# Kernel optimization log

Hardware: AMD Instinct MI355X
Metric: run time of the kernel (lower is better)

## Reference

```python
import jax, jax.numpy as jnp
import numpy as np

EMBED_DIM = 1024
NUM_HEADS = 16
HEAD_DIM = EMBED_DIM // NUM_HEADS


def setup_inputs() -> dict:
    key = jax.random.key(0)
    k1, k2, k3, k4, k5 = jax.random.split(key, 5)
    s = 1.0 / np.sqrt(EMBED_DIM)
    return {
        "query": jax.random.normal(k1, (8, 1024, EMBED_DIM), dtype=jnp.float32),
        "w_qkv": jax.random.normal(k2, (EMBED_DIM, 3 * EMBED_DIM), dtype=jnp.float32) * s,
        "b_qkv": jax.random.normal(k3, (3 * EMBED_DIM,), dtype=jnp.float32) * 0.01,
        "w_proj": jax.random.normal(k4, (EMBED_DIM, EMBED_DIM), dtype=jnp.float32) * s,
        "b_proj": jax.random.normal(k5, (EMBED_DIM,), dtype=jnp.float32) * 0.01,
    }


def reference(query, w_qkv, b_qkv, w_proj, b_proj):
    B, S, D = query.shape
    H, Hd = NUM_HEADS, HEAD_DIM
    scale = 1.0 / jnp.sqrt(jnp.asarray(Hd, query.dtype))
    # fused QKV projection; key=value=query (self-attention), so one GEMM suffices
    qkv = query @ w_qkv + b_qkv                      # [B, S, 3D]
    qkv = qkv.reshape(B, S, 3, H, Hd)
    q = qkv[:, :, 0].transpose(0, 2, 1, 3)           # [B, H, S, Hd]
    k = qkv[:, :, 1].transpose(0, 2, 1, 3)
    v = qkv[:, :, 2].transpose(0, 2, 1, 3)
    attn = jnp.einsum("bhqd,bhkd->bhqk", q, k) * scale
    attn = jax.nn.softmax(attn, axis=-1)
    out = jnp.einsum("bhqk,bhkd->bhqd", attn, v)     # [B, H, S, Hd]
    out = out.transpose(0, 2, 1, 3).reshape(B, S, D)
    return out @ w_proj + b_proj
```

## Files before the change

### kernel.cpp

```cpp
#include <hip/hip_runtime.h>
#include <stdint.h>

#define DEV __device__ __forceinline__

typedef short bf16x8 __attribute__((ext_vector_type(8)));
typedef float f32x4 __attribute__((ext_vector_type(4)));
typedef float f32x16 __attribute__((ext_vector_type(16)));
typedef unsigned u32x2 __attribute__((ext_vector_type(2)));

DEV short f2bf(float f) {
  uint32_t x = __builtin_bit_cast(uint32_t, f);
  uint32_t r = x + 0x7fffu + ((x >> 16) & 1u);
  return (short)(r >> 16);
}

DEV unsigned cvtpk(float lo, float hi) {
  unsigned r;
  asm("v_cvt_pk_bf16_f32 %0, %1, %2" : "=v"(r) : "v"(lo), "v"(hi));
  return r;
}
DEV void pswap(unsigned& a, unsigned& b) {
  asm("v_permlane32_swap_b32 %0, %1" : "+v"(a), "+v"(b));
}

DEV void gld16(const short* g, short* l) {
  __builtin_amdgcn_global_load_lds(
      (const __attribute__((address_space(1))) void*)g,
      (__attribute__((address_space(3))) void*)l, 16, 0, 0);
}

__global__ __launch_bounds__(256) void k_cvt(const float* __restrict__ in,
                                             short* __restrict__ out, int n8) {
  int i = blockIdx.x * 256 + threadIdx.x;
  if (i >= n8) return;
  const float4* p = (const float4*)in + (size_t)i * 2;
  float4 a = p[0], b = p[1];
  bf16x8 v;
  v[0] = f2bf(a.x); v[1] = f2bf(a.y); v[2] = f2bf(a.z); v[3] = f2bf(a.w);
  v[4] = f2bf(b.x); v[5] = f2bf(b.y); v[6] = f2bf(b.z); v[7] = f2bf(b.w);
  *(bf16x8*)(out + (size_t)i * 8) = v;
}

__global__ __launch_bounds__(256) void k_tcvt(const float* __restrict__ in,
                                              short* __restrict__ out, int K, int N) {
  __shared__ float tile[64][65];
  int t = threadIdx.x;
  int n0 = blockIdx.x * 64, k0 = blockIdx.y * 64;
  int kl = t >> 4, nl = (t & 15) * 4;
#pragma unroll
  for (int it = 0; it < 4; ++it) {
    float4 v = *(const float4*)&in[(size_t)(k0 + kl + it * 16) * N + n0 + nl];
    tile[nl + 0][kl + it * 16] = v.x;
    tile[nl + 1][kl + it * 16] = v.y;
    tile[nl + 2][kl + it * 16] = v.z;
    tile[nl + 3][kl + it * 16] = v.w;
  }
  __syncthreads();
  int no = t >> 2, kc = (t & 3) * 16;
  bf16x8 v0, v1;
#pragma unroll
  for (int c = 0; c < 8; ++c) v0[c] = f2bf(tile[no][kc + c]);
#pragma unroll
  for (int c = 0; c < 8; ++c) v1[c] = f2bf(tile[no][kc + 8 + c]);
  size_t ob = (size_t)(n0 + no) * K + k0 + kc;
  *(bf16x8*)&out[ob] = v0;
  *(bf16x8*)&out[ob + 8] = v1;
}

__global__ __launch_bounds__(256) void k_vt(const short* __restrict__ vin,
                                            short* __restrict__ vt) {
  __shared__ alignas(16) short tile[64][72];
  int t = threadIdx.x;
  int sc = blockIdx.x, bh = blockIdx.y;
  int sl = t >> 3, dc = (t & 7) * 8;
  const short* base = vin + ((size_t)bh * 1024 + sc * 64) * 64;
#pragma unroll
  for (int it = 0; it < 2; ++it)
    *(bf16x8*)&tile[sl + it * 32][dc] = *(const bf16x8*)&base[(size_t)(sl + it * 32) * 64 + dc];
  __syncthreads();
  int d = t >> 2, s2 = (t & 3) * 16;
  bf16x8 v0, v1;
#pragma unroll
  for (int c = 0; c < 8; ++c) v0[c] = tile[s2 + c][d];
#pragma unroll
  for (int c = 0; c < 8; ++c) v1[c] = tile[s2 + 8 + c][d];
  size_t ob = (size_t)bh * 65536 + (size_t)d * 1024 + sc * 64 + s2;
  *(bf16x8*)&vt[ob] = v0;
  *(bf16x8*)&vt[ob + 8] = v1;
}

template <int MODE, int BN>
__global__ __launch_bounds__(256) void k_gemm(const short* __restrict__ A,
                                              const short* __restrict__ Bw,
                                              const float* __restrict__ bias,
                                              void* o0, void* o1, void* o2) {
  constexpr int JN = BN / 32;
  __shared__ alignas(16) short lA[128 * 64];
  __shared__ alignas(16) short lB[BN * 64];
  int t = threadIdx.x;
  int w = t >> 6, l = t & 63;
  int wr = w >> 1, wc = w & 1;
  int lr = l & 15, lg = l >> 4;

  int nbx = gridDim.x;
  int flat = blockIdx.y * nbx + blockIdx.x;
  int tot = nbx * gridDim.y;
  int swz = (flat & 7) * (tot >> 3) + (flat >> 3);
  int m0 = (swz / nbx) * 128, n0 = (swz % nbx) * BN;

  f32x4 acc[4][JN] = {};

  int srow = t >> 3;
  int schunk = (t & 7) ^ (srow & 7);
  const short* ap = A + (size_t)(m0 + srow) * 1024 + schunk * 8;
  const short* bp = Bw + (size_t)(n0 + srow) * 1024 + schunk * 8;
  short* la0 = &lA[w * 512];
  short* lb0 = &lB[w * 512];

  for (int k0 = 0; k0 < 1024; k0 += 64) {
#pragma unroll
    for (int c = 0; c < 4; ++c)
      gld16(ap + (size_t)c * 32 * 1024 + k0, la0 + c * 2048);
#pragma unroll
    for (int c = 0; c < JN; ++c)
      gld16(bp + (size_t)c * 32 * 1024 + k0, lb0 + c * 2048);
    __syncthreads();
    bf16x8 af[4][2], bfr[JN][2];
#pragma unroll
    for (int i = 0; i < 4; ++i)
#pragma unroll
      for (int ks = 0; ks < 2; ++ks) {
        int ra = wr * 64 + i * 16 + lr;
        af[i][ks] = *(const bf16x8*)&lA[ra * 64 + (((ks * 4 + lg) ^ (ra & 7)) * 8)];
      }
#pragma unroll
    for (int j = 0; j < JN; ++j)
#pragma unroll
      for (int ks = 0; ks < 2; ++ks) {
        int rb = wc * (BN / 2) + j * 16 + lr;
        bfr[j][ks] = *(const bf16x8*)&lB[rb * 64 + (((ks * 4 + lg) ^ (rb & 7)) * 8)];
      }
#pragma unroll
    for (int i = 0; i < 4; ++i)
#pragma unroll
      for (int j = 0; j < JN; ++j)
#pragma unroll
        for (int ks = 0; ks < 2; ++ks)
          acc[i][j] = __builtin_amdgcn_mfma_f32_16x16x32_bf16(af[i][ks], bfr[j][ks], acc[i][j], 0, 0, 0);
    __syncthreads();
  }

  if (MODE == 0) {
    short* outs[3] = {(short*)o0, (short*)o1, (short*)o2};
#pragma unroll
    for (int i = 0; i < 4; ++i)
#pragma unroll
      for (int j = 0; j < JN; ++j) {
        int nn0 = n0 + wc * (BN / 2) + j * 16;
        int sel = nn0 >> 10;
        short* op = outs[sel];
        float qs = (sel == 0) ? 0.18033688011112042f : 1.0f;
#pragma unroll
        for (int r = 0; r < 4; ++r) {
          int mm = m0 + wr * 64 + i * 16 + lg * 4 + r;
          int nn = nn0 + lr;
          float val = (acc[i][j][r] + bias[nn]) * qs;
          int hh = (nn >> 6) & 15, dd = nn & 63;
          int bb = mm >> 10, ss = mm & 1023;
          op[((size_t)(bb * 16 + hh) * 1024 + ss) * 64 + dd] = f2bf(val);
        }
      }
  } else {
    float* op = (float*)o0;
#pragma unroll
    for (int i = 0; i < 4; ++i)
#pragma unroll
      for (int j = 0; j < JN; ++j)
#pragma unroll
        for (int r = 0; r < 4; ++r) {
          int mm = m0 + wr * 64 + i * 16 + lg * 4 + r;
          int nn = n0 + wc * (BN / 2) + j * 16 + lr;
          op[(size_t)mm * 1024 + nn] = acc[i][j][r] + bias[nn];
        }
  }
}

__global__ __launch_bounds__(256, 4) void k_attn(const short* __restrict__ qb,
                                                 const short* __restrict__ kb,
                                                 const short* __restrict__ vt,
                                                 short* __restrict__ ao) {
  __shared__ alignas(16) short lds[2 * 8192];
  int t = threadIdx.x, w = t >> 6, l = t & 63;
  int r0 = l & 31, hi = l >> 5;

  int bid = blockIdx.x;
  int swz = (bid & 7) * 128 + (bid >> 3);
  int bh = swz >> 3, qc = swz & 7;
  int q0 = qc * 128 + w * 32;

  const short* qbase = qb + (size_t)bh * 65536;
  const short* kbase = kb + (size_t)bh * 65536;
  const short* vbase = vt + (size_t)bh * 65536;

  bf16x8 qf[4];
#pragma unroll
  for (int step = 0; step < 4; ++step)
    qf[step] = *(const bf16x8*)&qbase[(size_t)(q0 + r0) * 64 + step * 16 + hi * 8];

  f32x16 acc0 = {0,0,0,0,0,0,0,0,0,0,0,0,0,0,0,0};
  f32x16 acc1 = {0,0,0,0,0,0,0,0,0,0,0,0,0,0,0,0};
  float ls = 0.f;

  int srow = t >> 3;
  int sch = (t & 7) ^ (srow & 7);
  const short* kp = kbase + (size_t)srow * 64 + sch * 8;
  const short* vp = vbase + (size_t)srow * 1024 + sch * 8;

#define STAGE(buf, kv0)                                              \
  do {                                                               \
    short* dk = &lds[(buf) * 8192 + w * 512];                        \
    short* dv = &lds[(buf) * 8192 + 4096 + w * 512];                 \
    gld16(kp + (size_t)(kv0) * 64, dk);                              \
    gld16(kp + (size_t)((kv0) + 32) * 64, dk + 2048);                \
    gld16(vp + (kv0), dv);                                           \
    gld16(vp + (kv0) + 32 * 1024, dv + 2048);                        \
  } while (0)

  STAGE(0, 0);
  int cur = 0;
  for (int it = 0; it < 16; ++it) {
    __syncthreads();
    if (it < 15) STAGE(cur ^ 1, (it + 1) * 64);
    const short* lk = &lds[cur * 8192];
    const short* lv = &lds[cur * 8192 + 4096];

    f32x16 s0 = {0,0,0,0,0,0,0,0,0,0,0,0,0,0,0,0};
    f32x16 s1 = {0,0,0,0,0,0,0,0,0,0,0,0,0,0,0,0};
    __builtin_amdgcn_s_setprio(1);
#pragma unroll
    for (int step = 0; step < 4; ++step) {
      int ck = step * 2 + hi;
      bf16x8 kf0 = *(const bf16x8*)&lk[r0 * 64 + ((ck ^ (r0 & 7)) * 8)];
      int r1 = 32 + r0;
      bf16x8 kf1 = *(const bf16x8*)&lk[r1 * 64 + ((ck ^ (r1 & 7)) * 8)];
      s0 = __builtin_amdgcn_mfma_f32_32x32x16_bf16(kf0, qf[step], s0, 0, 0, 0);
      s1 = __builtin_amdgcn_mfma_f32_32x32x16_bf16(kf1, qf[step], s1, 0, 0, 0);
    }
    __builtin_amdgcn_s_setprio(0);

    float rs = 0.f;
#pragma unroll
    for (int r = 0; r < 16; ++r) { float p = __builtin_exp2f(s0[r]); s0[r] = p; rs += p; }
#pragma unroll
    for (int r = 0; r < 16; ++r) { float p = __builtin_exp2f(s1[r]); s1[r] = p; rs += p; }
    rs += __shfl_xor(rs, 32);
    ls += rs;

    __builtin_amdgcn_s_setprio(1);
#pragma unroll
    for (int tt = 0; tt < 2; ++tt) {
#pragma unroll
      for (int ks = 0; ks < 2; ++ks) {
        unsigned Aw, Bw2, Cw, Dw;
        if (tt == 0) {
          Aw = cvtpk(s0[8 * ks + 0], s0[8 * ks + 1]);
          Bw2 = cvtpk(s0[8 * ks + 4], s0[8 * ks + 5]);
          Cw = cvtpk(s0[8 * ks + 2], s0[8 * ks + 3]);
          Dw = cvtpk(s0[8 * ks + 6], s0[8 * ks + 7]);
        } else {
          Aw = cvtpk(s1[8 * ks + 0], s1[8 * ks + 1]);
          Bw2 = cvtpk(s1[8 * ks + 4], s1[8 * ks + 5]);
          Cw = cvtpk(s1[8 * ks + 2], s1[8 * ks + 3]);
          Dw = cvtpk(s1[8 * ks + 6], s1[8 * ks + 7]);
        }
        pswap(Aw, Bw2);
        pswap(Cw, Dw);
        union { unsigned u[4]; bf16x8 v; } pb;
        pb.u[0] = Aw; pb.u[1] = Cw; pb.u[2] = Bw2; pb.u[3] = Dw;
        int cv = tt * 4 + ks * 2 + hi;
        bf16x8 vf0 = *(const bf16x8*)&lv[r0 * 64 + ((cv ^ (r0 & 7)) * 8)];
        int r1 = 32 + r0;
        bf16x8 vf1 = *(const bf16x8*)&lv[r1 * 64 + ((cv ^ (r1 & 7)) * 8)];
        acc0 = __builtin_amdgcn_mfma_f32_32x32x16_bf16(vf0, pb.v, acc0, 0, 0, 0);
        acc1 = __builtin_amdgcn_mfma_f32_32x32x16_bf16(vf1, pb.v, acc1, 0, 0, 0);
      }
    }
    __builtin_amdgcn_s_setprio(0);
    cur ^= 1;
  }
#undef STAGE

  __syncthreads();
  short* ep = &lds[w * 2048];
  float inv = 1.0f / ls;
#pragma unroll
  for (int d0 = 0; d0 < 2; ++d0) {
#pragma unroll
    for (int q4 = 0; q4 < 4; ++q4) {
      unsigned w0, w1;
      if (d0 == 0) {
        w0 = cvtpk(acc0[q4 * 4 + 0] * inv, acc0[q4 * 4 + 1] * inv);
        w1 = cvtpk(acc0[q4 * 4 + 2] * inv, acc0[q4 * 4 + 3] * inv);
      } else {
        w0 = cvtpk(acc1[q4 * 4 + 0] * inv, acc1[q4 * 4 + 1] * inv);
        w1 = cvtpk(acc1[q4 * 4 + 2] * inv, acc1[q4 * 4 + 3] * inv);
      }
      int chunk = (q4 + 4 * d0) ^ (r0 & 7);
      u32x2 uv; uv[0] = w0; uv[1] = w1;
      *(u32x2*)((char*)ep + r0 * 128 + chunk * 16 + hi * 8) = uv;
    }
  }
  int b = bh >> 4, hh = bh & 15;
#pragma unroll
  for (int rr = 0; rr < 4; ++rr) {
    int row = (l >> 3) + rr * 8;
    int c = (l & 7) ^ (row & 7);
    bf16x8 ov = *(const bf16x8*)((char*)ep + row * 128 + c * 16);
    int tok = b * 1024 + q0 + row;
    *(bf16x8*)&ao[(size_t)tok * 1024 + hh * 64 + (l & 7) * 8] = ov;
  }
}

extern "C" void kernel_launch(void* const* d_in, const int* in_sizes, int n_in,
                              void* d_out, int out_size, void* d_ws, size_t ws_size,
                              hipStream_t stream) {
  const float* query  = (const float*)d_in[0];
  const float* w_qkv  = (const float*)d_in[1];
  const float* b_qkv  = (const float*)d_in[2];
  const float* w_proj = (const float*)d_in[3];
  const float* b_proj = (const float*)d_in[4];
  float* out = (float*)d_out;
  char* ws = (char*)d_ws;

  short* qbf = (short*)(ws);
  short* wT  = (short*)(ws + 16777216);
  short* wpT = (short*)(ws + 23068672);
  short* qb  = (short*)(ws + 25165824);
  short* kb  = (short*)(ws + 41943040);
  short* vb  = (short*)(ws + 58720256);
  short* vt  = (short*)(ws + 75497472);
  short* ao  = qbf;

  k_cvt<<<4096, 256, 0, stream>>>(query, qbf, 1048576);
  k_tcvt<<<dim3(48, 16), 256, 0, stream>>>(w_qkv, wT, 1024, 3072);
  k_tcvt<<<dim3(16, 16), 256, 0, stream>>>(w_proj, wpT, 1024, 1024);
  k_gemm<0, 96><<<dim3(32, 64), 256, 0, stream>>>(qbf, wT, b_qkv, qb, kb, vb);
  k_vt<<<dim3(16, 128), 256, 0, stream>>>(vb, vt);
  k_attn<<<1024, 256, 0, stream>>>(qb, kb, vt, ao);
  k_gemm<1, 128><<<dim3(8, 64), 256, 0, stream>>>(ao, wpT, b_proj, out, nullptr, nullptr);
}
```

Baseline: 178.8 us.

## Replace QKV GEMM with 256x256-tile 8-wave double-buffered pipelined kernel

Adds a new QKV projection kernel that uses 256x256 output tiles, 512 threads (8 waves) and double-buffered LDS. Global-to-LDS loads for the next K tile are interleaved with four MFMA phases, using explicit waitcnt, barriers and setprio. The larger tile increases operand reuse per byte loaded and the schedule is meant to hide load latency. The cost is 128KB of LDS per block, heavy register pressure from 128 accumulators, a smaller grid of 384 blocks, and a scalar bf16 epilogue store scattered per element.

```diff
diff --git a/kernel.cpp b/kernel.cpp
--- a/kernel.cpp
+++ b/kernel.cpp
@@ -87,6 +87,137 @@
   size_t ob = (size_t)bh * 65536 + (size_t)d * 1024 + sc * 64 + s2;
   *(bf16x8*)&vt[ob] = v0;
   *(bf16x8*)&vt[ob + 8] = v1;
+}
+
+__global__ __launch_bounds__(512, 2) void k_g8(const short* __restrict__ A,
+                                               const short* __restrict__ Bw,
+                                               const float* __restrict__ bias,
+                                               short* __restrict__ oq,
+                                               short* __restrict__ ok,
+                                               short* __restrict__ ov) {
+  __shared__ alignas(16) short lA[2][16384];
+  __shared__ alignas(16) short lB[2][16384];
+  int t = threadIdx.x;
+  int w = t >> 6, l = t & 63;
+  int wr = w >> 2, wc = w & 3;
+  int lr = l & 15, lg = l >> 4;
+
+  int nbx = gridDim.x;
+  int flat = blockIdx.y * nbx + blockIdx.x;
+  int tot = nbx * gridDim.y;
+  int swz = (flat & 7) * (tot >> 3) + (flat >> 3);
+  int m0 = (swz / nbx) * 256, n0 = (swz % nbx) * 256;
+
+  f32x4 acc[8][4] = {};
+
+  int srow = t >> 3;
+  int schunk = (t & 7) ^ (srow & 7);
+  const short* ap = A + (size_t)(m0 + srow) * 1024 + schunk * 8;
+  const short* bp = Bw + (size_t)(n0 + srow) * 1024 + schunk * 8;
+  int lofs = w * 512;
+
+#define SA8(buf, kt, c) gld16(ap + (size_t)(c) * 65536 + (kt) * 64, &lA[buf][(c) * 4096 + lofs])
+#define SB8(buf, kt, c) gld16(bp + (size_t)(c) * 65536 + (kt) * 64, &lB[buf][(c) * 4096 + lofs])
+#define BAR8() do { __builtin_amdgcn_sched_barrier(0); __builtin_amdgcn_s_barrier(); \
+                    __builtin_amdgcn_sched_barrier(0); } while (0)
+#define LGKM0() do { asm volatile("s_waitcnt lgkmcnt(0)" ::: "memory"); \
+                     __builtin_amdgcn_sched_barrier(0); } while (0)
+
+  SB8(0, 0, 0); SB8(0, 0, 1); SB8(0, 0, 2); SB8(0, 0, 3);
+  SA8(0, 0, 0); SA8(0, 0, 2); SA8(0, 0, 1); SA8(0, 0, 3);
+  asm volatile("s_waitcnt vmcnt(2)" ::: "memory");
+  BAR8();
+
+#pragma unroll 2
+  for (int kt = 0; kt < 16; ++kt) {
+    int b = kt & 1;
+    const short* la = lA[b];
+    const short* lb = lB[b];
+    bool st = kt < 15;
+    bf16x8 bfr[4][2], af[2][2];
+
+#define DSREAD_A(p)                                                                     \
+    _Pragma("unroll") for (int i2 = 0; i2 < 2; ++i2)                                    \
+      _Pragma("unroll") for (int ks = 0; ks < 2; ++ks) {                                \
+        int ra = wr * 128 + ((p) * 2 + i2) * 16 + lr;                                   \
+        af[i2][ks] = *(const bf16x8*)&la[ra * 64 + (((ks * 4 + lg) ^ (ra & 7)) * 8)];   \
+      }
+#define MFMA16(p)                                                                       \
+    __builtin_amdgcn_s_setprio(1);                                                      \
+    _Pragma("unroll") for (int i2 = 0; i2 < 2; ++i2)                                    \
+      _Pragma("unroll") for (int nj = 0; nj < 4; ++nj)                                  \
+        _Pragma("unroll") for (int ks = 0; ks < 2; ++ks)                                \
+          acc[(p) * 2 + i2][nj] = __builtin_amdgcn_mfma_f32_16x16x32_bf16(              \
+              af[i2][ks], bfr[nj][ks], acc[(p) * 2 + i2][nj], 0, 0, 0);                 \
+    __builtin_amdgcn_s_setprio(0);
+
+#pragma unroll
+    for (int nj = 0; nj < 4; ++nj)
+#pragma unroll
+      for (int ks = 0; ks < 2; ++ks) {
+        int rb = wc * 64 + nj * 16 + lr;
+        bfr[nj][ks] = *(const bf16x8*)&lb[rb * 64 + (((ks * 4 + lg) ^ (rb & 7)) * 8)];
+      }
+    DSREAD_A(0)
+    if (st) { SB8(b ^ 1, kt + 1, 0); SB8(b ^ 1, kt + 1, 1); }
+    BAR8();
+    LGKM0();
+    MFMA16(0)
+    BAR8();
+
+    DSREAD_A(1)
+    if (st) {
+      SB8(b ^ 1, kt + 1, 2); SB8(b ^ 1, kt + 1, 3);
+      asm volatile("s_waitcnt vmcnt(4)" ::: "memory");
+    } else {
+      asm volatile("s_waitcnt vmcnt(0)" ::: "memory");
+    }
+    BAR8();
+    LGKM0();
+    MFMA16(1)
+    BAR8();
+
+    DSREAD_A(2)
+    if (st) { SA8(b ^ 1, kt + 1, 0); SA8(b ^ 1, kt + 1, 2); }
+    BAR8();
+    LGKM0();
+    MFMA16(2)
+    BAR8();
+
+    DSREAD_A(3)
+    if (st) {
+      SA8(b ^ 1, kt + 1, 1); SA8(b ^ 1, kt + 1, 3);
+      asm volatile("s_waitcnt vmcnt(2)" ::: "memory");
+    }
+    BAR8();
+    LGKM0();
+    MFMA16(3)
+    BAR8();
+#undef DSREAD_A
+#undef MFMA16
+  }
+#undef SA8
+#undef SB8
+
+  short* outs[3] = {oq, ok, ov};
+#pragma unroll
+  for (int mi = 0; mi < 8; ++mi)
+#pragma unroll
+    for (int nj = 0; nj < 4; ++nj) {
+      int nn0 = n0 + wc * 64 + nj * 16;
+      int sel = nn0 >> 10;
+      short* op = outs[sel];
+      float qs = (sel == 0) ? 0.18033688011112042f : 1.0f;
+#pragma unroll
+      for (int r = 0; r < 4; ++r) {
+        int mm = m0 + wr * 128 + mi * 16 + lg * 4 + r;
+        int nn = nn0 + lr;
+        float val = (acc[mi][nj][r] + bias[nn]) * qs;
+        int hh = (nn >> 6) & 15, dd = nn & 63;
+        int bb = mm >> 10, ss = mm & 1023;
+        op[((size_t)(bb * 16 + hh) * 1024 + ss) * 64 + dd] = f2bf(val);
+      }
+    }
 }
 
 template <int MODE, int BN>
@@ -344,7 +475,7 @@
   k_cvt<<<4096, 256, 0, stream>>>(query, qbf, 1048576);
   k_tcvt<<<dim3(48, 16), 256, 0, stream>>>(w_qkv, wT, 1024, 3072);
   k_tcvt<<<dim3(16, 16), 256, 0, stream>>>(w_proj, wpT, 1024, 1024);
-  k_gemm<0, 96><<<dim3(32, 64), 256, 0, stream>>>(qbf, wT, b_qkv, qb, kb, vb);
+  k_g8<<<dim3(12, 32), 512, 0, stream>>>(qbf, wT, b_qkv, qb, kb, vb);
   k_vt<<<dim3(16, 128), 256, 0, stream>>>(vb, vt);
   k_attn<<<1024, 256, 0, stream>>>(qb, kb, vt, ao);
   k_gemm<1, 128><<<dim3(8, 64), 256, 0, stream>>>(ao, wpT, b_proj, out, nullptr, nullptr);
```

New measurement: 182.9 us. 2.3% more time.

## Process two 32-row query tiles per wave in attention kernel with 128-thread blocks

Applied to the files above, without the earlier changes.

The attention block now uses 2 waves instead of 4, and each wave handles 64 query rows as two 32-row tiles. Each K/V fragment read from LDS then feeds twice as many MFMAs, which halves LDS read traffic per unit of compute. Each thread stages more K/V chunks per tile. The cost is roughly double the accumulator and score registers per wave, with fewer waves per block and lower occupancy, so less latency hiding.

```diff
diff --git a/kernel.cpp b/kernel.cpp
--- a/kernel.cpp
+++ b/kernel.cpp
@@ -185,7 +185,7 @@
   }
 }
 
-__global__ __launch_bounds__(256, 4) void k_attn(const short* __restrict__ qb,
+__global__ __launch_bounds__(128, 2) void k_attn(const short* __restrict__ qb,
                                                  const short* __restrict__ kb,
                                                  const short* __restrict__ vt,
                                                  short* __restrict__ ao) {
@@ -196,34 +196,36 @@
   int bid = blockIdx.x;
   int swz = (bid & 7) * 128 + (bid >> 3);
   int bh = swz >> 3, qc = swz & 7;
-  int q0 = qc * 128 + w * 32;
+  int q0 = qc * 128 + w * 64;
 
   const short* qbase = qb + (size_t)bh * 65536;
   const short* kbase = kb + (size_t)bh * 65536;
   const short* vbase = vt + (size_t)bh * 65536;
 
-  bf16x8 qf[4];
-#pragma unroll
-  for (int step = 0; step < 4; ++step)
-    qf[step] = *(const bf16x8*)&qbase[(size_t)(q0 + r0) * 64 + step * 16 + hi * 8];
-
-  f32x16 acc0 = {0,0,0,0,0,0,0,0,0,0,0,0,0,0,0,0};
-  f32x16 acc1 = {0,0,0,0,0,0,0,0,0,0,0,0,0,0,0,0};
-  float ls = 0.f;
-
-  int srow = t >> 3;
-  int sch = (t & 7) ^ (srow & 7);
+  bf16x8 qf[2][4];
+#pragma unroll
+  for (int qt = 0; qt < 2; ++qt)
+#pragma unroll
+    for (int step = 0; step < 4; ++step)
+      qf[qt][step] = *(const bf16x8*)&qbase[(size_t)(q0 + qt * 32 + r0) * 64 + step * 16 + hi * 8];
+
+  f32x16 acc[2][2] = {};
+  float ls[2] = {0.f, 0.f};
+
+  int srow = 32 * w + (l >> 3);
+  int sch = (l & 7) ^ (srow & 7);
   const short* kp = kbase + (size_t)srow * 64 + sch * 8;
   const short* vp = vbase + (size_t)srow * 1024 + sch * 8;
 
-#define STAGE(buf, kv0)                                              \
-  do {                                                               \
-    short* dk = &lds[(buf) * 8192 + w * 512];                        \
-    short* dv = &lds[(buf) * 8192 + 4096 + w * 512];                 \
-    gld16(kp + (size_t)(kv0) * 64, dk);                              \
-    gld16(kp + (size_t)((kv0) + 32) * 64, dk + 2048);                \
-    gld16(vp + (kv0), dv);                                           \
-    gld16(vp + (kv0) + 32 * 1024, dv + 2048);                        \
+#define STAGE(buf, kv0)                                                        \
+  do {                                                                         \
+    short* dk = &lds[(buf) * 8192 + w * 2048];                                 \
+    short* dv = &lds[(buf) * 8192 + 4096 + w * 2048];                          \
+    _Pragma("unroll")                                                          \
+    for (int c = 0; c < 4; ++c) {                                              \
+      gld16(kp + (size_t)((kv0) + 8 * c) * 64, dk + c * 512);                  \
+      gld16(vp + (kv0) + (size_t)(8 * c) * 1024, dv + c * 512);                \
+    }                                                                          \
   } while (0)
 
   STAGE(0, 0);
@@ -234,8 +236,7 @@
     const short* lk = &lds[cur * 8192];
     const short* lv = &lds[cur * 8192 + 4096];
 
-    f32x16 s0 = {0,0,0,0,0,0,0,0,0,0,0,0,0,0,0,0};
-    f32x16 s1 = {0,0,0,0,0,0,0,0,0,0,0,0,0,0,0,0};
+    f32x16 s0[2] = {}, s1[2] = {};
     __builtin_amdgcn_s_setprio(1);
 #pragma unroll
     for (int step = 0; step < 4; ++step) {
@@ -243,46 +244,55 @@
       bf16x8 kf0 = *(const bf16x8*)&lk[r0 * 64 + ((ck ^ (r0 & 7)) * 8)];
       int r1 = 32 + r0;
       bf16x8 kf1 = *(const bf16x8*)&lk[r1 * 64 + ((ck ^ (r1 & 7)) * 8)];
-      s0 = __builtin_amdgcn_mfma_f32_32x32x16_bf16(kf0, qf[step], s0, 0, 0, 0);
-      s1 = __builtin_amdgcn_mfma_f32_32x32x16_bf16(kf1, qf[step], s1, 0, 0, 0);
+#pragma unroll
+      for (int qt = 0; qt < 2; ++qt) {
+        s0[qt] = __builtin_amdgcn_mfma_f32_32x32x16_bf16(kf0, qf[qt][step], s0[qt], 0, 0, 0);
+        s1[qt] = __builtin_amdgcn_mfma_f32_32x32x16_bf16(kf1, qf[qt][step], s1[qt], 0, 0, 0);
+      }
     }
     __builtin_amdgcn_s_setprio(0);
 
-    float rs = 0.f;
-#pragma unroll
-    for (int r = 0; r < 16; ++r) { float p = __builtin_exp2f(s0[r]); s0[r] = p; rs += p; }
-#pragma unroll
-    for (int r = 0; r < 16; ++r) { float p = __builtin_exp2f(s1[r]); s1[r] = p; rs += p; }
-    rs += __shfl_xor(rs, 32);
-    ls += rs;
+#pragma unroll
+    for (int qt = 0; qt < 2; ++qt) {
+      float rs = 0.f;
+#pragma unroll
+      for (int r = 0; r < 16; ++r) { float p = __builtin_exp2f(s0[qt][r]); s0[qt][r] = p; rs += p; }
+#pragma unroll
+      for (int r = 0; r < 16; ++r) { float p = __builtin_exp2f(s1[qt][r]); s1[qt][r] = p; rs += p; }
+      rs += __shfl_xor(rs, 32);
+      ls[qt] += rs;
+    }
 
     __builtin_amdgcn_s_setprio(1);
 #pragma unroll
     for (int tt = 0; tt < 2; ++tt) {
 #pragma unroll
       for (int ks = 0; ks < 2; ++ks) {
-        unsigned Aw, Bw2, Cw, Dw;
-        if (tt == 0) {
-          Aw = cvtpk(s0[8 * ks + 0], s0[8 * ks + 1]);
-          Bw2 = cvtpk(s0[8 * ks + 4], s0[8 * ks + 5]);
-          Cw = cvtpk(s0[8 * ks + 2], s0[8 * ks + 3]);
-          Dw = cvtpk(s0[8 * ks + 6], s0[8 * ks + 7]);
-        } else {
-          Aw = cvtpk(s1[8 * ks + 0], s1[8 * ks + 1]);
-          Bw2 = cvtpk(s1[8 * ks + 4], s1[8 * ks + 5]);
-          Cw = cvtpk(s1[8 * ks + 2], s1[8 * ks + 3]);
-          Dw = cvtpk(s1[8 * ks + 6], s1[8 * ks + 7]);
-        }
-        pswap(Aw, Bw2);
-        pswap(Cw, Dw);
-        union { unsigned u[4]; bf16x8 v; } pb;
-        pb.u[0] = Aw; pb.u[1] = Cw; pb.u[2] = Bw2; pb.u[3] = Dw;
         int cv = tt * 4 + ks * 2 + hi;
         bf16x8 vf0 = *(const bf16x8*)&lv[r0 * 64 + ((cv ^ (r0 & 7)) * 8)];
         int r1 = 32 + r0;
         bf16x8 vf1 = *(const bf16x8*)&lv[r1 * 64 + ((cv ^ (r1 & 7)) * 8)];
-        acc0 = __builtin_amdgcn_mfma_f32_32x32x16_bf16(vf0, pb.v, acc0, 0, 0, 0);
-        acc1 = __builtin_amdgcn_mfma_f32_32x32x16_bf16(vf1, pb.v, acc1, 0, 0, 0);
+#pragma unroll
+        for (int qt = 0; qt < 2; ++qt) {
+          unsigned Aw, Bw2, Cw, Dw;
+          if (tt == 0) {
+            Aw = cvtpk(s0[qt][8 * ks + 0], s0[qt][8 * ks + 1]);
+            Bw2 = cvtpk(s0[qt][8 * ks + 4], s0[qt][8 * ks + 5]);
+            Cw = cvtpk(s0[qt][8 * ks + 2], s0[qt][8 * ks + 3]);
+            Dw = cvtpk(s0[qt][8 * ks + 6], s0[qt][8 * ks + 7]);
+          } else {
+            Aw = cvtpk(s1[qt][8 * ks + 0], s1[qt][8 * ks + 1]);
+            Bw2 = cvtpk(s1[qt][8 * ks + 4], s1[qt][8 * ks + 5]);
+            Cw = cvtpk(s1[qt][8 * ks + 2], s1[qt][8 * ks + 3]);
+            Dw = cvtpk(s1[qt][8 * ks + 6], s1[qt][8 * ks + 7]);
+          }
+          pswap(Aw, Bw2);
+          pswap(Cw, Dw);
+          union { unsigned u[4]; bf16x8 v; } pb;
+          pb.u[0] = Aw; pb.u[1] = Cw; pb.u[2] = Bw2; pb.u[3] = Dw;
+          acc[qt][0] = __builtin_amdgcn_mfma_f32_32x32x16_bf16(vf0, pb.v, acc[qt][0], 0, 0, 0);
+          acc[qt][1] = __builtin_amdgcn_mfma_f32_32x32x16_bf16(vf1, pb.v, acc[qt][1], 0, 0, 0);
+        }
       }
     }
     __builtin_amdgcn_s_setprio(0);
@@ -291,28 +301,32 @@
 #undef STAGE
 
   __syncthreads();
-  short* ep = &lds[w * 2048];
-  float inv = 1.0f / ls;
-#pragma unroll
-  for (int d0 = 0; d0 < 2; ++d0) {
-#pragma unroll
-    for (int q4 = 0; q4 < 4; ++q4) {
-      unsigned w0, w1;
-      if (d0 == 0) {
-        w0 = cvtpk(acc0[q4 * 4 + 0] * inv, acc0[q4 * 4 + 1] * inv);
-        w1 = cvtpk(acc0[q4 * 4 + 2] * inv, acc0[q4 * 4 + 3] * inv);
-      } else {
-        w0 = cvtpk(acc1[q4 * 4 + 0] * inv, acc1[q4 * 4 + 1] * inv);
-        w1 = cvtpk(acc1[q4 * 4 + 2] * inv, acc1[q4 * 4 + 3] * inv);
-      }
-      int chunk = (q4 + 4 * d0) ^ (r0 & 7);
-      u32x2 uv; uv[0] = w0; uv[1] = w1;
-      *(u32x2*)((char*)ep + r0 * 128 + chunk * 16 + hi * 8) = uv;
+  short* ep = &lds[w * 4096];
+#pragma unroll
+  for (int qt = 0; qt < 2; ++qt) {
+    float inv = 1.0f / ls[qt];
+    short* eq = ep + qt * 2048;
+#pragma unroll
+    for (int d0 = 0; d0 < 2; ++d0) {
+#pragma unroll
+      for (int q4 = 0; q4 < 4; ++q4) {
+        unsigned w0, w1;
+        if (d0 == 0) {
+          w0 = cvtpk(acc[qt][0][q4 * 4 + 0] * inv, acc[qt][0][q4 * 4 + 1] * inv);
+          w1 = cvtpk(acc[qt][0][q4 * 4 + 2] * inv, acc[qt][0][q4 * 4 + 3] * inv);
+        } else {
+          w0 = cvtpk(acc[qt][1][q4 * 4 + 0] * inv, acc[qt][1][q4 * 4 + 1] * inv);
+          w1 = cvtpk(acc[qt][1][q4 * 4 + 2] * inv, acc[qt][1][q4 * 4 + 3] * inv);
+        }
+        int chunk = (q4 + 4 * d0) ^ (r0 & 7);
+        u32x2 uv; uv[0] = w0; uv[1] = w1;
+        *(u32x2*)((char*)eq + r0 * 128 + chunk * 16 + hi * 8) = uv;
+      }
     }
   }
   int b = bh >> 4, hh = bh & 15;
 #pragma unroll
-  for (int rr = 0; rr < 4; ++rr) {
+  for (int rr = 0; rr < 8; ++rr) {
     int row = (l >> 3) + rr * 8;
     int c = (l & 7) ^ (row & 7);
     bf16x8 ov = *(const bf16x8*)((char*)ep + row * 128 + c * 16);
@@ -346,6 +360,6 @@
   k_tcvt<<<dim3(16, 16), 256, 0, stream>>>(w_proj, wpT, 1024, 1024);
   k_gemm<0, 96><<<dim3(32, 64), 256, 0, stream>>>(qbf, wT, b_qkv, qb, kb, vb);
   k_vt<<<dim3(16, 128), 256, 0, stream>>>(vb, vt);
-  k_attn<<<1024, 256, 0, stream>>>(qb, kb, vt, ao);
+  k_attn<<<1024, 128, 0, stream>>>(qb, kb, vt, ao);
   k_gemm<1, 128><<<dim3(8, 64), 256, 0, stream>>>(ao, wpT, b_proj, out, nullptr, nullptr);
 }
```

Measured after the change: 186.5 us. 4.3% more time.
